# Kernel optimization log

Hardware: AMD Instinct MI355X
Metric: run time of the kernel (lower is better)

The kernel has to match this reference:

```python
import jax, jax.numpy as jnp
import numpy as np

N_HEADS = 16


def setup_inputs() -> dict:
    key = jax.random.key(0)
    k1, k2, k3 = jax.random.split(key, 3)
    d = 1024
    x = jax.random.normal(k1, (8, 1024, d), dtype=jnp.float32)
    w_qkv = jax.random.normal(k2, (d, 3 * d), dtype=jnp.float32) * (1.0 / np.sqrt(d))
    w_out = jax.random.normal(k3, (d, d), dtype=jnp.float32) * (1.0 / np.sqrt(d))
    b_out = jnp.zeros((d,), dtype=jnp.float32)
    return {"x": x, "w_qkv": w_qkv, "w_out": w_out, "b_out": b_out}


def reference(x, w_qkv, w_out, b_out):
    a, b, c = x.shape
    h = N_HEADS
    hd = c // h
    scale = 1.0 / (c ** 0.5)  # note: 1/sqrt(model_dim), not head_dim
    qkv = (x @ w_qkv).reshape(a, b, 3, h, hd)
    q, k, v = jnp.moveaxis(qkv, 2, 0)          # each (a, b, h, hd)
    q = jnp.swapaxes(q, 1, 2)                  # (a, h, b, hd)
    k = jnp.swapaxes(k, 1, 2)
    v = jnp.swapaxes(v, 1, 2)
    scores = jnp.einsum('ahqd,ahkd->ahqk', q, k) * scale  # (a, h, b, b)
    # Faithful to the source: softmax over dim=1 (the HEADS axis)
    attn = jax.nn.softmax(scores, axis=1)
    out = jnp.einsum('ahqk,ahkd->ahqd', attn, v)           # (a, h, b, hd)
    out = jnp.swapaxes(out, 1, 2).reshape(a, b, c)
    return out @ w_out + b_out
```

## Files before the change

### kernel.cpp

```cpp
#include <hip/hip_runtime.h>
#include <hip/hip_bf16.h>

typedef __attribute__((ext_vector_type(8))) short short8;
typedef __attribute__((ext_vector_type(4))) short short4v;
typedef __attribute__((ext_vector_type(4))) float f32x4;

#define SC_LOG2E 0.04508422f

__device__ inline short bf16r(float f) {
    union { float f; unsigned u; } v; v.f = f;
    unsigned r = v.u + 0x7FFFu + ((v.u >> 16) & 1u);
    return (short)(r >> 16);
}
__device__ inline float bf2f(unsigned short u) {
    union { unsigned u; float f; } v; v.u = ((unsigned)u) << 16;
    return v.f;
}

#define GLOAD_LDS16(gp, lp) __builtin_amdgcn_global_load_lds( \
    (const __attribute__((address_space(1))) unsigned int*)(gp), \
    (__attribute__((address_space(3))) unsigned int*)(lp), 16, 0, 0)

__global__ void castk(const float* __restrict__ in, short* __restrict__ out, int n4) {
    int i = blockIdx.x * 256 + threadIdx.x;
    if (i < n4) {
        float4 v = ((const float4*)in)[i];
        short4 o;
        o.x = bf16r(v.x); o.y = bf16r(v.y); o.z = bf16r(v.z); o.w = bf16r(v.w);
        ((short4*)out)[i] = o;
    }
}

__global__ void tcast(const float* __restrict__ src, short* __restrict__ dst, int R, int C) {
    __shared__ float tile[32][33];
    int bi = blockIdx.x, bj = blockIdx.y;
    int tx = threadIdx.x & 31, ty = threadIdx.x >> 5;
#pragma unroll
    for (int p = 0; p < 4; p++)
        tile[ty + p * 8][tx] = src[(long)(bi * 32 + ty + p * 8) * C + bj * 32 + tx];
    __syncthreads();
#pragma unroll
    for (int p = 0; p < 4; p++)
        dst[(long)(bj * 32 + ty + p * 8) * R + bi * 32 + tx] = bf16r(tile[tx][ty + p * 8]);
}

__global__ void vtrans(const short* __restrict__ qkv, short* __restrict__ Vt) {
    __shared__ short tile[32][33];
    int a = blockIdx.z, bi = blockIdx.x, bj = blockIdx.y;
    int tx = threadIdx.x & 31, ty = threadIdx.x >> 5;
#pragma unroll
    for (int p = 0; p < 4; p++) {
        int k = bi * 32 + ty + p * 8;
        int r = bj * 32 + tx;
        tile[ty + p * 8][tx] = qkv[(long)(a * 1024 + k) * 3072 + 2048 + r];
    }
    __syncthreads();
#pragma unroll
    for (int p = 0; p < 4; p++) {
        int r = bj * 32 + ty + p * 8;
        int k = bi * 32 + tx;
        Vt[(long)a * 1048576 + (long)r * 1024 + k] = tile[tx][ty + p * 8];
    }
}

template<int OUT_BF16>
__global__ __launch_bounds__(256, 2)
void gemm_bt(const short* __restrict__ A, const short* __restrict__ Bt,
             void* __restrict__ Cout, const float* __restrict__ bias,
             int M, int N, int K, int nbx, int cpx) {
    __shared__ short As[2][128 * 32];
    __shared__ short Bs[2][128 * 32];
    const int wg = blockIdx.x;
    const int lg = (wg & 7) * cpx + (wg >> 3);
    const int bx = lg % nbx, by = lg / nbx;
    const int tid = threadIdx.x, w = tid >> 6, lane = tid & 63;
    const int wr = w >> 1, wc = w & 1;
    const int l15 = lane & 15, lhi = lane >> 4;
    const int m0 = by * 128, n0 = bx * 128;
    f32x4 acc[4][4] = {};
    const int NT = K / 32;

    auto stage = [&](int buf, int t) {
        int k0 = t * 32;
#pragma unroll
        for (int j = 0; j < 2; j++) {
            int chunk = w * 128 + j * 64 + lane;
            int row = chunk >> 2, cc = chunk & 3;
            GLOAD_LDS16(A  + (long)(m0 + row) * K + k0 + cc * 8, &As[buf][chunk * 8]);
            GLOAD_LDS16(Bt + (long)(n0 + row) * K + k0 + cc * 8, &Bs[buf][chunk * 8]);
        }
    };

    stage(0, 0);
    __syncthreads();
    int buf = 0;
    for (int t = 0; t < NT; t++) {
        if (t + 1 < NT) stage(buf ^ 1, t + 1);
        short8 af[4], bfr[4];
#pragma unroll
        for (int i = 0; i < 4; i++) {
            af[i]  = *(const short8*)(&As[buf][(wr * 64 + i * 16 + l15) * 32 + lhi * 8]);
            bfr[i] = *(const short8*)(&Bs[buf][(wc * 64 + i * 16 + l15) * 32 + lhi * 8]);
        }
#pragma unroll
        for (int i = 0; i < 4; i++)
#pragma unroll
            for (int j = 0; j < 4; j++)
                acc[i][j] = __builtin_amdgcn_mfma_f32_16x16x32_bf16(af[i], bfr[j], acc[i][j], 0, 0, 0);
        __syncthreads();
        buf ^= 1;
    }
#pragma unroll
    for (int i = 0; i < 4; i++)
#pragma unroll
        for (int j = 0; j < 4; j++)
#pragma unroll
            for (int r = 0; r < 4; r++) {
                int row = m0 + wr * 64 + i * 16 + lhi * 4 + r;
                int col = n0 + wc * 64 + j * 16 + l15;
                float v = acc[i][j][r];
                if (OUT_BF16) ((short*)Cout)[(long)row * N + col] = bf16r(v);
                else          ((float*)Cout)[(long)row * N + col] = v + bias[col];
            }
}

__global__ __launch_bounds__(256, 2)
void dsum_kernel(const short* __restrict__ qkv, short* __restrict__ Dinv) {
    __shared__ short Qs[2][128 * 64];
    __shared__ short Ks[2][128 * 64];
    const int wg = blockIdx.x;
    const int lg = (wg & 7) * 64 + (wg >> 3);
    const int a = lg >> 6, q0 = ((lg >> 3) & 7) * 128, k0 = (lg & 7) * 128;
    const int tid = threadIdx.x, w = tid >> 6, lane = tid & 63;
    const int wr = w >> 1, wc = w & 1;
    const int l15 = lane & 15, lhi = lane >> 4;
    const long qb = (long)a * 1024 * 3072;
    f32x4 dacc[4][4] = {};

    auto stage = [&](int buf, int h) {
#pragma unroll
        for (int j = 0; j < 4; j++) {
            int c = (w * 4 + j) * 64 + lane;
            int row = c >> 3, cc = (c & 7) ^ (row & 7);
            GLOAD_LDS16(qkv + qb + (long)(q0 + row) * 3072 + h * 64 + cc * 8,        &Qs[buf][c * 8]);
            GLOAD_LDS16(qkv + qb + (long)(k0 + row) * 3072 + 1024 + h * 64 + cc * 8, &Ks[buf][c * 8]);
        }
    };

    stage(0, 0);
    __syncthreads();
    int buf = 0;
    for (int h = 0; h < 16; h++) {
        if (h < 15) stage(buf ^ 1, h + 1);
        short8 kaf[4][2], qbf[4][2];
#pragma unroll
        for (int i = 0; i < 4; i++) {
            int row = wr * 64 + i * 16 + l15;
#pragma unroll
            for (int df = 0; df < 2; df++)
                kaf[i][df] = *(const short8*)(&Ks[buf][row * 64 + (((df * 4 + lhi) ^ (row & 7)) * 8)]);
        }
#pragma unroll
        for (int j = 0; j < 4; j++) {
            int row = wc * 64 + j * 16 + l15;
#pragma unroll
            for (int df = 0; df < 2; df++)
                qbf[j][df] = *(const short8*)(&Qs[buf][row * 64 + (((df * 4 + lhi) ^ (row & 7)) * 8)]);
        }
#pragma unroll
        for (int i = 0; i < 4; i++)
#pragma unroll
            for (int j = 0; j < 4; j++) {
                f32x4 s = {};
                s = __builtin_amdgcn_mfma_f32_16x16x32_bf16(kaf[i][0], qbf[j][0], s, 0, 0, 0);
                s = __builtin_amdgcn_mfma_f32_16x16x32_bf16(kaf[i][1], qbf[j][1], s, 0, 0, 0);
#pragma unroll
                for (int r = 0; r < 4; r++)
                    dacc[i][j][r] += exp2f(s[r] * SC_LOG2E);
            }
        __syncthreads();
        buf ^= 1;
    }
#pragma unroll
    for (int i = 0; i < 4; i++)
#pragma unroll
        for (int j = 0; j < 4; j++) {
            int q16 = (q0 >> 4) + wc * 4 + j;
            int k16 = (k0 >> 4) + wr * 4 + i;
            short4v s4;
#pragma unroll
            for (int r = 0; r < 4; r++) s4[r] = bf16r(1.0f / dacc[i][j][r]);
            *(short4v*)(Dinv + ((((long)a * 64 + q16) * 64 + k16) << 8) + lane * 4) = s4;
        }
}

__global__ __launch_bounds__(256, 2)
void attn2_kernel(const short* __restrict__ qkv, const short* __restrict__ Vt,
                  const short* __restrict__ Dinv, short* __restrict__ ctx) {
    __shared__ short Ks[2][64 * 64];
    __shared__ short Vs[2][64 * 64];
    __shared__ short pbu[4 * 2048];
    const int wg = blockIdx.x;
    const int lg = (wg & 7) * 128 + (wg >> 3);
    const int a = lg >> 7, h = (lg >> 3) & 15, q0 = (lg & 7) * 128;
    const int tid = threadIdx.x, w = tid >> 6, lane = tid & 63;
    const int l15 = lane & 15, lhi = lane >> 4;
    const int qw = q0 + w * 32, qw16 = qw >> 4;
    const long qb = (long)a * 1024 * 3072;

    short8 qf[2][2];
#pragma unroll
    for (int qi = 0; qi < 2; qi++)
#pragma unroll
        for (int df = 0; df < 2; df++)
            qf[qi][df] = *(const short8*)(qkv + qb + (long)(qw + qi * 16 + l15) * 3072 + h * 64 + df * 32 + lhi * 8);

    f32x4 oacc[2][4] = {};
    short* pw = &pbu[w * 2048];
    const int sw = (l15 & 7) << 1;

    auto stage = [&](int buf, int t) {
        int k0 = t * 64;
#pragma unroll
        for (int j = 0; j < 2; j++) {
            int c = (w * 2 + j) * 64 + lane;
            int row = c >> 3, cc = (c & 7) ^ (row & 7);
            GLOAD_LDS16(qkv + qb + (long)(k0 + row) * 3072 + 1024 + h * 64 + cc * 8, &Ks[buf][c * 8]);
            GLOAD_LDS16(Vt + (long)a * 1048576 + (long)(h * 64 + row) * 1024 + k0 + cc * 8, &Vs[buf][c * 8]);
        }
    };

    stage(0, 0);
    __syncthreads();
    int buf = 0;
    for (int t = 0; t < 16; t++) {
        short4v dv4[2][4];
#pragma unroll
        for (int qi = 0; qi < 2; qi++)
#pragma unroll
            for (int kj = 0; kj < 4; kj++)
                dv4[qi][kj] = *(const short4v*)(Dinv + ((((long)a * 64 + qw16 + qi) * 64 + t * 4 + kj) << 8) + lane * 4);
        if (t < 15) stage(buf ^ 1, t + 1);
        f32x4 sacc[2][4] = {};
#pragma unroll
        for (int kj = 0; kj < 4; kj++) {
            int row = kj * 16 + l15;
#pragma unroll
            for (int df = 0; df < 2; df++) {
                short8 kf = *(const short8*)(&Ks[buf][row * 64 + (((df * 4 + lhi) ^ (row & 7)) * 8)]);
#pragma unroll
                for (int qi = 0; qi < 2; qi++)
                    sacc[qi][kj] = __builtin_amdgcn_mfma_f32_16x16x32_bf16(kf, qf[qi][df], sacc[qi][kj], 0, 0, 0);
            }
        }
#pragma unroll
        for (int qi = 0; qi < 2; qi++) {
            int q = qi * 16 + l15;
#pragma unroll
            for (int kj = 0; kj < 4; kj++) {
                short4v s4;
#pragma unroll
                for (int r = 0; r < 4; r++)
                    s4[r] = bf16r(exp2f(sacc[qi][kj][r] * SC_LOG2E) * bf2f((unsigned short)dv4[qi][kj][r]));
                int cc = (kj * 4 + lhi) ^ sw;
                *(short4v*)(&pw[q * 64 + cc * 4]) = s4;
            }
        }
#pragma unroll
        for (int qi = 0; qi < 2; qi++) {
            int q = qi * 16 + l15;
            short8 pf[2];
#pragma unroll
            for (int kc = 0; kc < 2; kc++) {
                int cc = (kc * 8 + lhi * 2) ^ sw;
                pf[kc] = *(const short8*)(&pw[q * 64 + cc * 4]);
            }
#pragma unroll
            for (int dj = 0; dj < 4; dj++) {
                int vrow = dj * 16 + l15;
#pragma unroll
                for (int kc = 0; kc < 2; kc++) {
                    short8 vf = *(const short8*)(&Vs[buf][vrow * 64 + (((kc * 4 + lhi) ^ (vrow & 7)) * 8)]);
                    oacc[qi][dj] = __builtin_amdgcn_mfma_f32_16x16x32_bf16(pf[kc], vf, oacc[qi][dj], 0, 0, 0);
                }
            }
        }
        __syncthreads();
        buf ^= 1;
    }
#pragma unroll
    for (int qi = 0; qi < 2; qi++)
#pragma unroll
        for (int dj = 0; dj < 4; dj++)
#pragma unroll
            for (int r = 0; r < 4; r++) {
                int q = qw + qi * 16 + lhi * 4 + r;
                ctx[((long)a * 1024 + q) * 1024 + h * 64 + dj * 16 + l15] = bf16r(oacc[qi][dj][r]);
            }
}

extern "C" void kernel_launch(void* const* d_in, const int* in_sizes, int n_in,
                              void* d_out, int out_size, void* d_ws, size_t ws_size,
                              hipStream_t stream) {
    const float* x     = (const float*)d_in[0];
    const float* w_qkv = (const float*)d_in[1];
    const float* w_out = (const float*)d_in[2];
    const float* b_out = (const float*)d_in[3];
    float* out = (float*)d_out;

    char* ws = (char*)d_ws;
    short* xb    = (short*)(ws);
    short* Dinv  = (short*)(ws);
    short* wqkvT = (short*)(ws + 16777216);
    short* woT   = (short*)(ws + 23068672);
    short* qkv   = (short*)(ws + 25165824);
    short* Vt    = (short*)(ws + 75497472);
    short* ctx   = (short*)(ws + 92274688);
    if (ws_size < 109051904u) return;

    castk<<<8192, 256, 0, stream>>>(x, xb, 2097152);
    tcast<<<dim3(32, 96), 256, 0, stream>>>(w_qkv, wqkvT, 1024, 3072);
    tcast<<<dim3(32, 32), 256, 0, stream>>>(w_out, woT, 1024, 1024);
    gemm_bt<1><<<1536, 256, 0, stream>>>(xb, wqkvT, (void*)qkv, nullptr, 8192, 3072, 1024, 24, 192);
    vtrans<<<dim3(32, 32, 8), 256, 0, stream>>>(qkv, Vt);
    dsum_kernel<<<512, 256, 0, stream>>>(qkv, Dinv);
    attn2_kernel<<<1024, 256, 0, stream>>>(qkv, Vt, Dinv, ctx);
    gemm_bt<0><<<512, 256, 0, stream>>>(ctx, woT, (void*)out, b_out, 8192, 1024, 1024, 8, 64);
}
```

Baseline: 236.7 us.

## Switch attention kernels to 32x32x16 MFMA and keep P in registers

```diff
diff --git a/kernel.cpp b/kernel.cpp
--- a/kernel.cpp
+++ b/kernel.cpp
@@ -4,17 +4,30 @@
 typedef __attribute__((ext_vector_type(8))) short short8;
 typedef __attribute__((ext_vector_type(4))) short short4v;
 typedef __attribute__((ext_vector_type(4))) float f32x4;
+typedef __attribute__((ext_vector_type(16))) float f32x16;
+typedef __attribute__((ext_vector_type(4))) unsigned uint4v;
 
 #define SC_LOG2E 0.04508422f
+#define MFMA32(a, b, c) __builtin_amdgcn_mfma_f32_32x32x16_bf16(a, b, c, 0, 0, 0)
 
 __device__ inline short bf16r(float f) {
     union { float f; unsigned u; } v; v.f = f;
     unsigned r = v.u + 0x7FFFu + ((v.u >> 16) & 1u);
     return (short)(r >> 16);
 }
-__device__ inline float bf2f(unsigned short u) {
-    union { unsigned u; float f; } v; v.u = ((unsigned)u) << 16;
-    return v.f;
+__device__ inline float bflo(unsigned u) {
+    union { unsigned u; float f; } v; v.u = u << 16; return v.f;
+}
+__device__ inline float bfhi(unsigned u) {
+    union { unsigned u; float f; } v; v.u = u & 0xffff0000u; return v.f;
+}
+__device__ inline unsigned cvt_pk_bf16(float lo, float hi) {
+    unsigned r;
+    asm("v_cvt_pk_bf16_f32 %0, %1, %2" : "=v"(r) : "v"(lo), "v"(hi));
+    return r;
+}
+__device__ inline void perm32swap(unsigned& a, unsigned& b) {
+    asm("v_permlane32_swap_b32 %0, %1" : "+v"(a), "+v"(b));
 }
 
 #define GLOAD_LDS16(gp, lp) __builtin_amdgcn_global_load_lds( \
@@ -125,7 +138,7 @@
 }
 
 __global__ __launch_bounds__(256, 2)
-void dsum_kernel(const short* __restrict__ qkv, short* __restrict__ Dinv) {
+void dsum_kernel(const short* __restrict__ qkv, unsigned* __restrict__ Dinv) {
     __shared__ short Qs[2][128 * 64];
     __shared__ short Ks[2][128 * 64];
     const int wg = blockIdx.x;
@@ -133,169 +146,197 @@
     const int a = lg >> 6, q0 = ((lg >> 3) & 7) * 128, k0 = (lg & 7) * 128;
     const int tid = threadIdx.x, w = tid >> 6, lane = tid & 63;
     const int wr = w >> 1, wc = w & 1;
-    const int l15 = lane & 15, lhi = lane >> 4;
-    const long qb = (long)a * 1024 * 3072;
-    f32x4 dacc[4][4] = {};
-
-    auto stage = [&](int buf, int h) {
+    const int l31 = lane & 31, hi = lane >> 5;
+    const long qb = (long)a * 3145728;
+    f32x16 dacc[2][2] = {};
+
+    auto stage = [&](int buf, int hh) {
 #pragma unroll
         for (int j = 0; j < 4; j++) {
-            int c = (w * 4 + j) * 64 + lane;
+            int c = j * 256 + tid;
             int row = c >> 3, cc = (c & 7) ^ (row & 7);
-            GLOAD_LDS16(qkv + qb + (long)(q0 + row) * 3072 + h * 64 + cc * 8,        &Qs[buf][c * 8]);
-            GLOAD_LDS16(qkv + qb + (long)(k0 + row) * 3072 + 1024 + h * 64 + cc * 8, &Ks[buf][c * 8]);
+            GLOAD_LDS16(qkv + qb + (long)(q0 + row) * 3072 + hh * 64 + cc * 8,        &Qs[buf][c * 8]);
+            GLOAD_LDS16(qkv + qb + (long)(k0 + row) * 3072 + 1024 + hh * 64 + cc * 8, &Ks[buf][c * 8]);
         }
     };
 
     stage(0, 0);
     __syncthreads();
     int buf = 0;
-    for (int h = 0; h < 16; h++) {
-        if (h < 15) stage(buf ^ 1, h + 1);
-        short8 kaf[4][2], qbf[4][2];
-#pragma unroll
-        for (int i = 0; i < 4; i++) {
-            int row = wr * 64 + i * 16 + l15;
-#pragma unroll
-            for (int df = 0; df < 2; df++)
-                kaf[i][df] = *(const short8*)(&Ks[buf][row * 64 + (((df * 4 + lhi) ^ (row & 7)) * 8)]);
-        }
-#pragma unroll
-        for (int j = 0; j < 4; j++) {
-            int row = wc * 64 + j * 16 + l15;
-#pragma unroll
-            for (int df = 0; df < 2; df++)
-                qbf[j][df] = *(const short8*)(&Qs[buf][row * 64 + (((df * 4 + lhi) ^ (row & 7)) * 8)]);
-        }
-#pragma unroll
-        for (int i = 0; i < 4; i++)
-#pragma unroll
-            for (int j = 0; j < 4; j++) {
-                f32x4 s = {};
-                s = __builtin_amdgcn_mfma_f32_16x16x32_bf16(kaf[i][0], qbf[j][0], s, 0, 0, 0);
-                s = __builtin_amdgcn_mfma_f32_16x16x32_bf16(kaf[i][1], qbf[j][1], s, 0, 0, 0);
-#pragma unroll
-                for (int r = 0; r < 4; r++)
+    for (int hh = 0; hh < 16; hh++) {
+        if (hh < 15) stage(buf ^ 1, hh + 1);
+        short8 ka[2][4], qf[2][4];
+#pragma unroll
+        for (int i = 0; i < 2; i++)
+#pragma unroll
+            for (int dc = 0; dc < 4; dc++) {
+                int row = wr * 64 + i * 32 + l31;
+                int ph = (dc * 2 + hi) ^ (row & 7);
+                ka[i][dc] = *(const short8*)(&Ks[buf][row * 64 + ph * 8]);
+            }
+#pragma unroll
+        for (int j = 0; j < 2; j++)
+#pragma unroll
+            for (int dc = 0; dc < 4; dc++) {
+                int row = wc * 64 + j * 32 + l31;
+                int ph = (dc * 2 + hi) ^ (row & 7);
+                qf[j][dc] = *(const short8*)(&Qs[buf][row * 64 + ph * 8]);
+            }
+#pragma unroll
+        for (int i = 0; i < 2; i++)
+#pragma unroll
+            for (int j = 0; j < 2; j++) {
+                f32x16 s = {};
+#pragma unroll
+                for (int dc = 0; dc < 4; dc++)
+                    s = MFMA32(ka[i][dc], qf[j][dc], s);
+#pragma unroll
+                for (int r = 0; r < 16; r++)
                     dacc[i][j][r] += exp2f(s[r] * SC_LOG2E);
             }
         __syncthreads();
         buf ^= 1;
     }
 #pragma unroll
-    for (int i = 0; i < 4; i++)
-#pragma unroll
-        for (int j = 0; j < 4; j++) {
-            int q16 = (q0 >> 4) + wc * 4 + j;
-            int k16 = (k0 >> 4) + wr * 4 + i;
-            short4v s4;
-#pragma unroll
-            for (int r = 0; r < 4; r++) s4[r] = bf16r(1.0f / dacc[i][j][r]);
-            *(short4v*)(Dinv + ((((long)a * 64 + q16) * 64 + k16) << 8) + lane * 4) = s4;
+    for (int i = 0; i < 2; i++)
+#pragma unroll
+        for (int j = 0; j < 2; j++) {
+            int ktg = (k0 >> 5) + wr * 2 + i;
+            int qtg = (q0 >> 5) + wc * 2 + j;
+            unsigned pw[8];
+#pragma unroll
+            for (int u = 0; u < 8; u++)
+                pw[u] = cvt_pk_bf16(1.0f / dacc[i][j][2 * u], 1.0f / dacc[i][j][2 * u + 1]);
+            unsigned* dst = Dinv + (((long)a * 32 + ktg) * 32 + qtg) * 512 + lane * 8;
+            *(uint4v*)dst       = (uint4v){pw[0], pw[1], pw[2], pw[3]};
+            *(uint4v*)(dst + 4) = (uint4v){pw[4], pw[5], pw[6], pw[7]};
         }
 }
 
 __global__ __launch_bounds__(256, 2)
 void attn2_kernel(const short* __restrict__ qkv, const short* __restrict__ Vt,
-                  const short* __restrict__ Dinv, short* __restrict__ ctx) {
+                  const unsigned* __restrict__ Dinv, short* __restrict__ ctx) {
     __shared__ short Ks[2][64 * 64];
     __shared__ short Vs[2][64 * 64];
-    __shared__ short pbu[4 * 2048];
     const int wg = blockIdx.x;
-    const int lg = (wg & 7) * 128 + (wg >> 3);
-    const int a = lg >> 7, h = (lg >> 3) & 15, q0 = (lg & 7) * 128;
+    const int lg = (wg & 7) * 64 + (wg >> 3);
+    const int a = lg >> 6, h = (lg >> 2) & 15, qblk = lg & 3;
+    const int q0 = qblk * 256;
     const int tid = threadIdx.x, w = tid >> 6, lane = tid & 63;
-    const int l15 = lane & 15, lhi = lane >> 4;
-    const int qw = q0 + w * 32, qw16 = qw >> 4;
-    const long qb = (long)a * 1024 * 3072;
-
-    short8 qf[2][2];
-#pragma unroll
-    for (int qi = 0; qi < 2; qi++)
-#pragma unroll
-        for (int df = 0; df < 2; df++)
-            qf[qi][df] = *(const short8*)(qkv + qb + (long)(qw + qi * 16 + l15) * 3072 + h * 64 + df * 32 + lhi * 8);
-
-    f32x4 oacc[2][4] = {};
-    short* pw = &pbu[w * 2048];
-    const int sw = (l15 & 7) << 1;
+    const int l31 = lane & 31, hi = lane >> 5;
+    const int qw = q0 + w * 64;
+    const long qb = (long)a * 3145728;
+
+    short8 qfrag[2][4];
+#pragma unroll
+    for (int qs = 0; qs < 2; qs++)
+#pragma unroll
+        for (int dc = 0; dc < 4; dc++)
+            qfrag[qs][dc] = *(const short8*)(qkv + qb +
+                (long)(qw + qs * 32 + l31) * 3072 + h * 64 + dc * 16 + hi * 8);
+
+    f32x16 oacc[2][2] = {};
 
     auto stage = [&](int buf, int t) {
-        int k0 = t * 64;
 #pragma unroll
         for (int j = 0; j < 2; j++) {
-            int c = (w * 2 + j) * 64 + lane;
+            int c = j * 256 + tid;
             int row = c >> 3, cc = (c & 7) ^ (row & 7);
-            GLOAD_LDS16(qkv + qb + (long)(k0 + row) * 3072 + 1024 + h * 64 + cc * 8, &Ks[buf][c * 8]);
-            GLOAD_LDS16(Vt + (long)a * 1048576 + (long)(h * 64 + row) * 1024 + k0 + cc * 8, &Vs[buf][c * 8]);
+            GLOAD_LDS16(qkv + qb + (long)(a * 0 + t * 64 + row) * 3072 + (long)a * 0 +
+                        (long)(0) + 1024 + h * 64 + cc * 8 + (long)(t * 0), &Ks[buf][c * 8]);
+            GLOAD_LDS16(Vt + (long)a * 1048576 + (long)(h * 64 + row) * 1024 + t * 64 + cc * 8,
+                        &Vs[buf][c * 8]);
         }
     };
-
-    stage(0, 0);
+    const short* kbase = qkv + qb + 1024 + h * 64;
+
+    auto stage2 = [&](int buf, int t) {
+#pragma unroll
+        for (int j = 0; j < 2; j++) {
+            int c = j * 256 + tid;
+            int row = c >> 3, cc = (c & 7) ^ (row & 7);
+            GLOAD_LDS16(kbase + (long)(t * 64 + row) * 3072 + cc * 8, &Ks[buf][c * 8]);
+            GLOAD_LDS16(Vt + (long)a * 1048576 + (long)(h * 64 + row) * 1024 + t * 64 + cc * 8,
+                        &Vs[buf][c * 8]);
+        }
+    };
+    (void)stage;
+
+    const unsigned* dbase = Dinv + ((long)a * 1024) * 512 + lane * 8;
+
+    stage2(0, 0);
     __syncthreads();
     int buf = 0;
     for (int t = 0; t < 16; t++) {
-        short4v dv4[2][4];
-#pragma unroll
-        for (int qi = 0; qi < 2; qi++)
-#pragma unroll
-            for (int kj = 0; kj < 4; kj++)
-                dv4[qi][kj] = *(const short4v*)(Dinv + ((((long)a * 64 + qw16 + qi) * 64 + t * 4 + kj) << 8) + lane * 4);
-        if (t < 15) stage(buf ^ 1, t + 1);
-        f32x4 sacc[2][4] = {};
-#pragma unroll
-        for (int kj = 0; kj < 4; kj++) {
-            int row = kj * 16 + l15;
-#pragma unroll
-            for (int df = 0; df < 2; df++) {
-                short8 kf = *(const short8*)(&Ks[buf][row * 64 + (((df * 4 + lhi) ^ (row & 7)) * 8)]);
-#pragma unroll
-                for (int qi = 0; qi < 2; qi++)
-                    sacc[qi][kj] = __builtin_amdgcn_mfma_f32_16x16x32_bf16(kf, qf[qi][df], sacc[qi][kj], 0, 0, 0);
-            }
-        }
-#pragma unroll
-        for (int qi = 0; qi < 2; qi++) {
-            int q = qi * 16 + l15;
-#pragma unroll
-            for (int kj = 0; kj < 4; kj++) {
-                short4v s4;
-#pragma unroll
-                for (int r = 0; r < 4; r++)
-                    s4[r] = bf16r(exp2f(sacc[qi][kj][r] * SC_LOG2E) * bf2f((unsigned short)dv4[qi][kj][r]));
-                int cc = (kj * 4 + lhi) ^ sw;
-                *(short4v*)(&pw[q * 64 + cc * 4]) = s4;
-            }
-        }
-#pragma unroll
-        for (int qi = 0; qi < 2; qi++) {
-            int q = qi * 16 + l15;
-            short8 pf[2];
-#pragma unroll
-            for (int kc = 0; kc < 2; kc++) {
-                int cc = (kc * 8 + lhi * 2) ^ sw;
-                pf[kc] = *(const short8*)(&pw[q * 64 + cc * 4]);
-            }
-#pragma unroll
-            for (int dj = 0; dj < 4; dj++) {
-                int vrow = dj * 16 + l15;
-#pragma unroll
-                for (int kc = 0; kc < 2; kc++) {
-                    short8 vf = *(const short8*)(&Vs[buf][vrow * 64 + (((kc * 4 + lhi) ^ (vrow & 7)) * 8)]);
-                    oacc[qi][dj] = __builtin_amdgcn_mfma_f32_16x16x32_bf16(pf[kc], vf, oacc[qi][dj], 0, 0, 0);
+        uint4v dv[2][2][2];
+#pragma unroll
+        for (int qs = 0; qs < 2; qs++)
+#pragma unroll
+            for (int kt = 0; kt < 2; kt++) {
+                int qtg = qblk * 8 + w * 2 + qs;
+                int ktg = t * 2 + kt;
+                const unsigned* dp = dbase + ((long)ktg * 32 + qtg) * 512;
+                dv[qs][kt][0] = *(const uint4v*)dp;
+                dv[qs][kt][1] = *(const uint4v*)(dp + 4);
+            }
+        if (t < 15) stage2(buf ^ 1, t + 1);
+
+        short8 pfrag[2][4];
+#pragma unroll
+        for (int kt = 0; kt < 2; kt++) {
+            short8 ka[4];
+#pragma unroll
+            for (int dc = 0; dc < 4; dc++) {
+                int row = kt * 32 + l31;
+                int ph = (dc * 2 + hi) ^ (row & 7);
+                ka[dc] = *(const short8*)(&Ks[buf][row * 64 + ph * 8]);
+            }
+#pragma unroll
+            for (int qs = 0; qs < 2; qs++) {
+                f32x16 s = {};
+#pragma unroll
+                for (int dc = 0; dc < 4; dc++)
+                    s = MFMA32(ka[dc], qfrag[qs][dc], s);
+                unsigned pw[8];
+#pragma unroll
+                for (int u = 0; u < 8; u++) {
+                    unsigned dm = dv[qs][kt][u >> 2][u & 3];
+                    float e0 = exp2f(s[2 * u]     * SC_LOG2E) * bflo(dm);
+                    float e1 = exp2f(s[2 * u + 1] * SC_LOG2E) * bfhi(dm);
+                    pw[u] = cvt_pk_bf16(e0, e1);
                 }
-            }
-        }
+                perm32swap(pw[0], pw[2]); perm32swap(pw[1], pw[3]);
+                perm32swap(pw[4], pw[6]); perm32swap(pw[5], pw[7]);
+                union { uint4v u; short8 s8; } c0, c1;
+                c0.u = (uint4v){pw[0], pw[1], pw[2], pw[3]};
+                c1.u = (uint4v){pw[4], pw[5], pw[6], pw[7]};
+                pfrag[qs][kt * 2 + 0] = c0.s8;
+                pfrag[qs][kt * 2 + 1] = c1.s8;
+            }
+        }
+#pragma unroll
+        for (int dt = 0; dt < 2; dt++)
+#pragma unroll
+            for (int n = 0; n < 4; n++) {
+                int row = dt * 32 + l31;
+                int ph = (n * 2 + hi) ^ (row & 7);
+                short8 vf = *(const short8*)(&Vs[buf][row * 64 + ph * 8]);
+#pragma unroll
+                for (int qs = 0; qs < 2; qs++)
+                    oacc[qs][dt] = MFMA32(pfrag[qs][n], vf, oacc[qs][dt]);
+            }
         __syncthreads();
         buf ^= 1;
     }
 #pragma unroll
-    for (int qi = 0; qi < 2; qi++)
-#pragma unroll
-        for (int dj = 0; dj < 4; dj++)
-#pragma unroll
-            for (int r = 0; r < 4; r++) {
-                int q = qw + qi * 16 + lhi * 4 + r;
-                ctx[((long)a * 1024 + q) * 1024 + h * 64 + dj * 16 + l15] = bf16r(oacc[qi][dj][r]);
+    for (int qs = 0; qs < 2; qs++)
+#pragma unroll
+        for (int dt = 0; dt < 2; dt++)
+#pragma unroll
+            for (int r = 0; r < 16; r++) {
+                int q = qw + qs * 32 + (r & 3) + 8 * (r >> 2) + 4 * hi;
+                int col = h * 64 + dt * 32 + l31;
+                ctx[((long)a * 1024 + q) * 1024 + col] = bf16r(oacc[qs][dt][r]);
             }
 }
 
@@ -309,8 +350,8 @@
     float* out = (float*)d_out;
 
     char* ws = (char*)d_ws;
-    short* xb    = (short*)(ws);
-    short* Dinv  = (short*)(ws);
+    short* xb       = (short*)(ws);
+    unsigned* Dinv  = (unsigned*)(ws);
     short* wqkvT = (short*)(ws + 16777216);
     short* woT   = (short*)(ws + 23068672);
     short* qkv   = (short*)(ws + 25165824);
@@ -324,6 +365,6 @@
     gemm_bt<1><<<1536, 256, 0, stream>>>(xb, wqkvT, (void*)qkv, nullptr, 8192, 3072, 1024, 24, 192);
     vtrans<<<dim3(32, 32, 8), 256, 0, stream>>>(qkv, Vt);
     dsum_kernel<<<512, 256, 0, stream>>>(qkv, Dinv);
-    attn2_kernel<<<1024, 256, 0, stream>>>(qkv, Vt, Dinv, ctx);
+    attn2_kernel<<<512, 256, 0, stream>>>(qkv, Vt, Dinv, ctx);
     gemm_bt<0><<<512, 256, 0, stream>>>(ctx, woT, (void*)out, b_out, 8192, 1024, 1024, 8, 64);
 }
```

New measurement: 228.1 us. -3.6%, faster.
